# Kernel optimization log

Hardware: AMD Instinct MI355X
Metric: run time of the kernel (lower is better)

The kernel has to match this reference:

```python
import jax, jax.numpy as jnp
import numpy as np

B, S, T, D, K = 8, 500, 30, 5, 10
H, TW, E = 64, 512, 8000


def gru_scan(x, Wi, Wh, bi, bh, lengths=None):
    """Torch-convention GRU. x: [N,T,Din] -> (full [N,T,H], last [N,H]).
    If lengths is given, hidden state freezes past each sequence's length and
    padded steps of `full` are zeroed."""
    N, Tn, _ = x.shape
    Hh = Wh.shape[0]
    xg = jnp.moveaxis(x @ Wi + bi, 1, 0)  # [T,N,3H]

    def step(h, inp):
        xg_t, t = inp
        hg = h @ Wh + bh
        xr, xz, xn = jnp.split(xg_t, 3, axis=-1)
        hr, hz, hn = jnp.split(hg, 3, axis=-1)
        r = jax.nn.sigmoid(xr + hr)
        z = jax.nn.sigmoid(xz + hz)
        n = jnp.tanh(xn + r * hn)
        h_new = (1.0 - z) * n + z * h
        if lengths is not None:
            valid = (t < lengths)[:, None]
            h_new = jnp.where(valid, h_new, h)
            full_t = jnp.where(valid, h_new, 0.0)
        else:
            full_t = h_new
        return h_new, full_t

    h0 = jnp.zeros((N, Hh), x.dtype)
    last, full = jax.lax.scan(step, h0, (xg, jnp.arange(Tn)))
    return jnp.moveaxis(full, 0, 1), last


def layer_norm(x, g, b, eps=1e-5):
    m = jnp.mean(x, axis=-1, keepdims=True)
    v = jnp.var(x, axis=-1, keepdims=True)
    return (x - m) / jnp.sqrt(v + eps) * g + b


def setup_inputs() -> dict:
    key = jax.random.key(0)
    ks = jax.random.split(key, 40)
    p = lambda i, shape: jax.random.normal(ks[i], shape, jnp.float32) * 0.05
    inp = {}
    inp['price'] = jax.random.normal(ks[0], (B, S, T, 3), jnp.float32)
    inp['tweets'] = jax.random.normal(ks[1], (B, S, D, K, TW), jnp.float32)
    inp['tweet_counts'] = jax.random.randint(ks[2], (B, S, D), 0, K + 1, jnp.int32)
    inp['edge_index'] = jax.random.randint(ks[3], (2, E), 0, S, jnp.int32)
    inp['num_edge_type'] = 3
    # price GRU (in=3)
    inp['pg_Wi'] = p(4, (3, 3 * H)); inp['pg_Wh'] = p(5, (H, 3 * H))
    inp['pg_bi'] = p(6, (3 * H,)); inp['pg_bh'] = p(7, (3 * H,))
    # tweet GRU (in=512)
    inp['tg_Wi'] = p(8, (TW, 3 * H)); inp['tg_Wh'] = p(9, (H, 3 * H))
    inp['tg_bi'] = p(10, (3 * H,)); inp['tg_bh'] = p(11, (3 * H,))
    # date GRU (in=64)
    inp['dg_Wi'] = p(12, (H, 3 * H)); inp['dg_Wh'] = p(13, (H, 3 * H))
    inp['dg_bi'] = p(14, (3 * H,)); inp['dg_bh'] = p(15, (3 * H,))
    inp['bil_A'] = p(16, (H, H, H)); inp['bil_b'] = p(17, (H,))
    inp['gnn_W'] = p(18, (H, H)); inp['gnn_b'] = p(19, (H,))
    inp['fc1_W'] = p(20, (2 * H, H)); inp['fc1_b'] = p(21, (H,))
    inp['ln1_g'] = jnp.ones((H,), jnp.float32); inp['ln1_b'] = jnp.zeros((H,), jnp.float32)
    inp['fc2_W'] = p(22, (H, H)); inp['fc2_b'] = p(23, (H,))
    inp['ln2_g'] = jnp.ones((H,), jnp.float32); inp['ln2_b'] = jnp.zeros((H,), jnp.float32)
    inp['mlp_W1'] = p(24, (H, H)); inp['mlp_b1'] = p(25, (H,))
    inp['mlp_W2'] = p(26, (H, 1)); inp['mlp_b2'] = p(27, (1,))
    return inp


def reference(price, tweets, pg_Wi, pg_Wh, pg_bi, pg_bh,
              tg_Wi, tg_Wh, tg_bi, tg_bh, dg_Wi, dg_Wh, dg_bi, dg_bh,
              bil_A, bil_b, gnn_W, gnn_b, fc1_W, fc1_b, ln1_g, ln1_b,
              fc2_W, fc2_b, ln2_g, ln2_b, mlp_W1, mlp_b1, mlp_W2, mlp_b2,
              tweet_counts, edge_index, num_edge_type):
    # NOTE: in the original, attn applies softmax over dim=1 of a [T,1] score,
    # i.e. a size-1 axis, so the weights are identically 1 and the attention
    # context is exactly sum(full, axis=0). We reproduce that exact math.
    # Price branch: GRU over T days for every (window, stock), then masked sum.
    pf, _ = gru_scan(price.reshape(B * S, T, 3), pg_Wi, pg_Wh, pg_bi, pg_bh)
    x = pf.sum(axis=1)  # [B*S, H]

    # Tweet branch: ragged GRU over up to K tweets per (window, stock, date).
    tw = tweets.reshape(B * S * D, K, TW)
    lens = tweet_counts.reshape(B * S * D)
    tf, _ = gru_scan(tw, tg_Wi, tg_Wh, tg_bi, tg_bh, lengths=lens)
    news = tf.sum(axis=1).reshape(B * S, D, H)  # zeros where count==0

    # Date GRU over the D daily news vectors.
    df, _ = gru_scan(news, dg_Wi, dg_Wh, dg_bi, dg_bh)
    text = df.sum(axis=1)  # [B*S, H]

    # Bilinear fusion: out_k = text A_k x + b_k, then tanh.
    comb = jnp.tanh(jnp.einsum('ni,kij,nj->nk', text, bil_A, x) + bil_b)
    ft = comb.reshape(B, S, H)

    # Simple GNN: mean-aggregate neighbor features over edge list, then linear.
    src, dst = edge_index[0], edge_index[1]
    deg = jax.ops.segment_sum(jnp.ones((E,), ft.dtype), dst, num_segments=S)
    denom = jnp.maximum(deg, 1.0)[:, None]
    agg = jax.vmap(lambda m: jax.ops.segment_sum(m, dst, num_segments=S))(ft[:, src, :])
    g = jnp.tanh((agg / denom) @ gnn_W + gnn_b)

    h = jnp.concatenate([ft, g], axis=-1)            # [B,S,2H]
    h = jax.nn.relu(layer_norm(h @ fc1_W + fc1_b, ln1_g, ln1_b))  # dropout: eval
    h = jax.nn.relu(layer_norm(h @ fc2_W + fc2_b, ln2_g, ln2_b))
    h = jax.nn.relu(h @ mlp_W1 + mlp_b1)
    logits = (h @ mlp_W2 + mlp_b2).reshape(B, S)
    return logits
```

## Files before the change

kernel.cpp:

```cpp
#include <hip/hip_runtime.h>
#include <math.h>

#define Bq 8
#define Sq 500
#define Tq 30
#define Dq 5
#define Kq 10
#define Hq 64
#define TWq 512
#define Eq 8000
#define NS (Bq*Sq)
#define NTt (NS*Dq)
#define G3 (3*Hq)
#define TG 4

#define MR 48
#define KC 64
#define XPITCH 72
#define XGP 196
#define NKT (TWq/32)
#define NNT (G3/16)
#define PSEQ 16

#define XROWS 40
#define STG_PLANE (MR*XPITCH)
#define STG_BUF  (2*STG_PLANE)

typedef __attribute__((ext_vector_type(8))) short short8_t;
typedef __attribute__((ext_vector_type(4))) float float4_t;

__device__ __forceinline__ float fsig(float x) {
    return 1.0f / (1.0f + __expf(-x));
}
__device__ __forceinline__ float ftanh(float x) {
    return 1.0f - 2.0f / (__expf(2.0f * x) + 1.0f);
}

__device__ __forceinline__ float wave_sum64(float v) {
    #pragma unroll
    for (int off = 32; off; off >>= 1) v += __shfl_xor(v, off, 64);
    return v;
}

__device__ __forceinline__ short f32_to_bf16_rn(float f) {
    union { float f; unsigned u; } v; v.f = f;
    unsigned r = v.u + 0x7fffu + ((v.u >> 16) & 1u);
    return (short)(r >> 16);
}
__device__ __forceinline__ float bf16_to_f32(short s) {
    union { unsigned u; float f; } v; v.u = ((unsigned)(unsigned short)s) << 16;
    return v.f;
}

__global__ __launch_bounds__(64)
void wfrag_prep_kernel(const float* __restrict__ Wi,
                       short* __restrict__ Wf_hi, short* __restrict__ Wf_lo) {
    const int kt = blockIdx.x / NNT;
    const int nt = blockIdx.x - kt*NNT;
    const int lane = threadIdx.x;
    const int quad = lane >> 4, l16 = lane & 15;
    short h[8], l[8];
    #pragma unroll
    for (int j = 0; j < 8; j++) {
        int k = kt*32 + quad*8 + j;
        int n = nt*16 + l16;
        float w = Wi[(size_t)k*G3 + n];
        short hi = f32_to_bf16_rn(w);
        short lo = f32_to_bf16_rn(w - bf16_to_f32(hi));
        h[j] = hi; l[j] = lo;
    }
    size_t off = ((size_t)blockIdx.x*64 + lane)*8;
    *(short8_t*)(Wf_hi + off) = *(const short8_t*)h;
    *(short8_t*)(Wf_lo + off) = *(const short8_t*)l;
}

__global__ __launch_bounds__(64)
void bilfrag_prep_kernel(const float* __restrict__ A,
                         short* __restrict__ Bf_hi, short* __restrict__ Bf_lo) {
    const int kt = blockIdx.x >> 2;
    const int nt = blockIdx.x & 3;
    const int lane = threadIdx.x;
    const int quad = lane >> 4, l16 = lane & 15;
    short h[8], l[8];
    #pragma unroll
    for (int j = 0; j < 8; j++) {
        int kidx = kt*32 + quad*8 + j;
        int n = nt*16 + l16;
        float w = A[(size_t)n*4096 + kidx];
        short hi = f32_to_bf16_rn(w);
        h[j] = hi; l[j] = f32_to_bf16_rn(w - bf16_to_f32(hi));
    }
    size_t off = ((size_t)blockIdx.x*64 + lane)*8;
    *(short8_t*)(Bf_hi + off) = *(const short8_t*)h;
    *(short8_t*)(Bf_lo + off) = *(const short8_t*)l;
}

__global__ __launch_bounds__(256)
void price_gru_mfma_kernel(const float* __restrict__ price,
                           const float* __restrict__ Wi,
                           const short* __restrict__ Whf_hi, const short* __restrict__ Whf_lo,
                           const float* __restrict__ bi, const float* __restrict__ bh,
                           float* __restrict__ xout) {
    __shared__ __align__(16) float price_s[PSEQ*90];
    __shared__ __align__(16) short h_hi[PSEQ*72];
    __shared__ __align__(16) short h_lo[PSEQ*72];
    const int tid = threadIdx.x;
    const int n0 = blockIdx.x * PSEQ;
    const int wv = tid >> 6;
    const int lane = tid & 63;
    const int quad = lane >> 4;
    const int l16 = lane & 15;
    const int u = wv*16 + l16;
    for (int i = tid; i < PSEQ*90; i += 256) price_s[i] = price[(size_t)n0*90 + i];
    for (int i = tid; i < PSEQ*72; i += 256) { h_hi[i] = 0; h_lo[i] = 0; }
    float wir[3], wiz[3], win[3];
    #pragma unroll
    for (int k = 0; k < 3; k++) {
        wir[k] = Wi[k*G3 + u];
        wiz[k] = Wi[k*G3 + 64 + u];
        win[k] = Wi[k*G3 + 128 + u];
    }
    const float cbr = bi[u] + bh[u];
    const float cbz = bi[64+u] + bh[64+u];
    const float bin = bi[128+u];
    const float bhn = bh[128+u];
    short8_t bfh[2][3], bfl[2][3];
    #pragma unroll
    for (int kt = 0; kt < 2; kt++)
        #pragma unroll
        for (int g = 0; g < 3; g++) {
            size_t off = (((size_t)kt*NNT + (g*4 + wv))*64 + lane)*8;
            bfh[kt][g] = *(const short8_t*)(Whf_hi + off);
            bfl[kt][g] = *(const short8_t*)(Whf_lo + off);
        }
    float hprev[4] = {0.f,0.f,0.f,0.f}, sum[4] = {0.f,0.f,0.f,0.f};
    __syncthreads();
    for (int t = 0; t < Tq; t++) {
        short8_t ah[2], al[2];
        #pragma unroll
        for (int kt = 0; kt < 2; kt++) {
            int addr = l16*72 + kt*32 + quad*8;
            ah[kt] = *(const short8_t*)&h_hi[addr];
            al[kt] = *(const short8_t*)&h_lo[addr];
        }
        float4_t accr = {0.f,0.f,0.f,0.f}, accz = {0.f,0.f,0.f,0.f}, accn = {0.f,0.f,0.f,0.f};
        #pragma unroll
        for (int kt = 0; kt < 2; kt++) {
            accr = __builtin_amdgcn_mfma_f32_16x16x32_bf16(ah[kt], bfh[kt][0], accr, 0,0,0);
            accr = __builtin_amdgcn_mfma_f32_16x16x32_bf16(ah[kt], bfl[kt][0], accr, 0,0,0);
            accr = __builtin_amdgcn_mfma_f32_16x16x32_bf16(al[kt], bfh[kt][0], accr, 0,0,0);
            accz = __builtin_amdgcn_mfma_f32_16x16x32_bf16(ah[kt], bfh[kt][1], accz, 0,0,0);
            accz = __builtin_amdgcn_mfma_f32_16x16x32_bf16(ah[kt], bfl[kt][1], accz, 0,0,0);
            accz = __builtin_amdgcn_mfma_f32_16x16x32_bf16(al[kt], bfh[kt][1], accz, 0,0,0);
            accn = __builtin_amdgcn_mfma_f32_16x16x32_bf16(ah[kt], bfh[kt][2], accn, 0,0,0);
            accn = __builtin_amdgcn_mfma_f32_16x16x32_bf16(ah[kt], bfl[kt][2], accn, 0,0,0);
            accn = __builtin_amdgcn_mfma_f32_16x16x32_bf16(al[kt], bfl[kt][2], accn, 0,0,0);
        }
        __syncthreads();
        #pragma unroll
        for (int r = 0; r < 4; r++) {
            const int s = quad*4 + r;
            float p0 = price_s[s*90 + t*3 + 0];
            float p1 = price_s[s*90 + t*3 + 1];
            float p2 = price_s[s*90 + t*3 + 2];
            float xr = fmaf(p2, wir[2], fmaf(p1, wir[1], fmaf(p0, wir[0], cbr)));
            float xz = fmaf(p2, wiz[2], fmaf(p1, wiz[1], fmaf(p0, wiz[0], cbz)));
            float xn = fmaf(p2, win[2], fmaf(p1, win[1], fmaf(p0, win[0], bin)));
            float rg = fsig(xr + accr[r]);
            float zg = fsig(xz + accz[r]);
            float ng = ftanh(xn + rg*(accn[r] + bhn));
            float h = (1.0f - zg)*ng + zg*hprev[r];
            hprev[r] = h; sum[r] += h;
            short hh = f32_to_bf16_rn(h);
            h_hi[s*72 + u] = hh;
            h_lo[s*72 + u] = f32_to_bf16_rn(h - bf16_to_f32(hh));
        }
        __syncthreads();
    }
    #pragma unroll
    for (int r = 0; r < 4; r++)
        xout[(size_t)(n0 + quad*4 + r)*Hq + u] = sum[r];
}

__global__ __launch_bounds__(256, 4)
void tweet_gru_kernel(const float* __restrict__ tweets,
                      const int* __restrict__ counts,
                      const short* __restrict__ Wf_hi, const short* __restrict__ Wf_lo,
                      const short* __restrict__ Wht_hi, const short* __restrict__ Wht_lo,
                      const float* __restrict__ bi, const float* __restrict__ bh,
                      float* __restrict__ news) {
    __shared__ __align__(16) char smem[XROWS*XGP*4];
    __shared__ __align__(16) short rh_hi[16*72];
    __shared__ __align__(16) short rh_lo[16*72];
    __shared__ int len_s[TG];
    __shared__ int tmax_s;
    short* stg = (short*)smem;
    float* xg  = (float*)smem;

    const int tid  = threadIdx.x;
    const int n0   = blockIdx.x * TG;
    const int wave = tid >> 6;
    const int lane = tid & 63;
    const int quad = lane >> 4;
    const int l16  = lane & 15;

    if (tid < TG) {
        int c = counts[n0 + tid];
        len_s[tid] = c < 0 ? 0 : (c > Kq ? Kq : c);
    }
    for (int i = tid; i < 16*72; i += 256) { rh_hi[i] = 0; rh_lo[i] = 0; }
    __syncthreads();
    if (tid == 0) {
        int m01 = len_s[0] > len_s[1] ? len_s[0] : len_s[1];
        int m23 = len_s[2] > len_s[3] ? len_s[2] : len_s[3];
        tmax_s = m01 > m23 ? m01 : m23;
    }

    const float* gp[3];
    int lofs[3];
    bool val[3];
    #pragma unroll
    for (int j = 0; j < 3; j++) {
        const int ii = tid + j*256;
        const bool ok = ii < TG*Kq*(KC/4);
        const int i = ok ? ii : 0;
        const int row = i >> 4;
        const int c4  = i & 15;
        const int s   = (row*205) >> 11;
        const int t   = row - s*10;
        val[j]  = ok && (t < len_s[s]);
        gp[j]   = tweets + (((size_t)(n0+s))*Kq + t)*TWq + c4*4;
        lofs[j] = row*XPITCH + c4*4;
    }

    float4_t acc[3][3];
    #pragma unroll
    for (int a = 0; a < 3; a++)
        #pragma unroll
        for (int b = 0; b < 3; b++)
            acc[a][b] = (float4_t){0.f, 0.f, 0.f, 0.f};

    #pragma unroll
    for (int j = 0; j < 3; j++) if (val[j]) {
        float4 v = *(const float4*)(gp[j]);
        float f[4] = {v.x, v.y, v.z, v.w};
        short hh[4], ll[4];
        #pragma unroll
        for (int q = 0; q < 4; q++) {
            short hi = f32_to_bf16_rn(f[q]);
            hh[q] = hi;
            ll[q] = f32_to_bf16_rn(f[q] - bf16_to_f32(hi));
        }
        *(short4*)&stg[lofs[j]]             = *(const short4*)hh;
        *(short4*)&stg[STG_PLANE + lofs[j]] = *(const short4*)ll;
    }
    __syncthreads();

    for (int ch = 0; ch < TWq/KC; ch++) {
        const int cur = ch & 1;
        float4 v[3];
        if (ch < TWq/KC - 1) {
            #pragma unroll
            for (int j = 0; j < 3; j++) if (val[j])
                v[j] = *(const float4*)(gp[j] + (ch+1)*KC);
        }
        const short* xh = stg + cur*STG_BUF;
        const short* xl = xh + STG_PLANE;
        #pragma unroll
        for (int ks = 0; ks < KC/32; ks++) {
            const int kt = ch*(KC/32) + ks;
            short8_t bh_[3], bl_[3];
            #pragma unroll
            for (int ntl = 0; ntl < 3; ntl++) {
                size_t off = (((size_t)kt*NNT + (wave*3 + ntl))*64 + lane)*8;
                bh_[ntl] = *(const short8_t*)(Wf_hi + off);
                bl_[ntl] = *(const short8_t*)(Wf_lo + off);
            }
            short8_t ah_[3], al_[3];
            #pragma unroll
            for (int mt = 0; mt < 3; mt++) {
                int addr = (mt*16 + l16)*XPITCH + ks*32 + quad*8;
                ah_[mt] = *(const short8_t*)&xh[addr];
                al_[mt] = *(const short8_t*)&xl[addr];
            }
            #pragma unroll
            for (int mt = 0; mt < 3; mt++)
                #pragma unroll
                for (int ntl = 0; ntl < 3; ntl++) {
                    acc[mt][ntl] = __builtin_amdgcn_mfma_f32_16x16x32_bf16(ah_[mt], bh_[ntl], acc[mt][ntl], 0, 0, 0);
                    acc[mt][ntl] = __builtin_amdgcn_mfma_f32_16x16x32_bf16(ah_[mt], bl_[ntl], acc[mt][ntl], 0, 0, 0);
                    acc[mt][ntl] = __builtin_amdgcn_mfma_f32_16x16x32_bf16(al_[mt], bh_[ntl], acc[mt][ntl], 0, 0, 0);
                }
        }
        if (ch < TWq/KC - 1) {
            short* yh = stg + (cur^1)*STG_BUF;
            short* yl = yh + STG_PLANE;
            #pragma unroll
            for (int j = 0; j < 3; j++) if (val[j]) {
                float f[4] = {v[j].x, v[j].y, v[j].z, v[j].w};
                short hh[4], ll[4];
                #pragma unroll
                for (int q = 0; q < 4; q++) {
                    short hi = f32_to_bf16_rn(f[q]);
                    hh[q] = hi;
                    ll[q] = f32_to_bf16_rn(f[q] - bf16_to_f32(hi));
                }
                *(short4*)&yh[lofs[j]] = *(const short4*)hh;
                *(short4*)&yl[lofs[j]] = *(const short4*)ll;
            }
        }
        __syncthreads();
    }

    #pragma unroll
    for (int ntl = 0; ntl < 3; ntl++) {
        const int col = (wave*3 + ntl)*16 + l16;
        const float bic = bi[col];
        #pragma unroll
        for (int mt = 0; mt < 3; mt++) {
            const int row0 = mt*16 + quad*4;
            if (row0 < XROWS) {
                #pragma unroll
                for (int r2 = 0; r2 < 4; r2++)
                    xg[(row0 + r2)*XGP + col] = acc[mt][ntl][r2] + bic;
            }
        }
    }

    const int u = wave*16 + l16;
    short8_t tbh[2][3], tbl[2][3];
    #pragma unroll
    for (int kt = 0; kt < 2; kt++)
        #pragma unroll
        for (int g = 0; g < 3; g++) {
            size_t off = (((size_t)kt*NNT + (g*4 + wave))*64 + lane)*8;
            tbh[kt][g] = *(const short8_t*)(Wht_hi + off);
            tbl[kt][g] = *(const short8_t*)(Wht_lo + off);
        }
    const float bhr = bh[u];
    const float bhz = bh[64+u];
    const float bhn = bh[128+u];
    int lp[4];
    #pragma unroll
    for (int r = 0; r < 4; r++) lp[r] = len_s[r];
    float hprev[4] = {0.f,0.f,0.f,0.f}, sum[4] = {0.f,0.f,0.f,0.f};
    const int tmax = tmax_s;
    for (int t = 0; t < tmax; t++) {
        const int ha = l16*72;
        short8_t ah0 = *(const short8_t*)&rh_hi[ha + quad*8];
        short8_t ah1 = *(const short8_t*)&rh_hi[ha + 32 + quad*8];
        short8_t al0 = *(const short8_t*)&rh_lo[ha + quad*8];
        short8_t al1 = *(const short8_t*)&rh_lo[ha + 32 + quad*8];
        float4_t ar = {0.f,0.f,0.f,0.f}, az = {0.f,0.f,0.f,0.f}, an = {0.f,0.f,0.f,0.f};
        ar = __builtin_amdgcn_mfma_f32_16x16x32_bf16(ah0, tbh[0][0], ar, 0,0,0);
        ar = __builtin_amdgcn_mfma_f32_16x16x32_bf16(ah0, tbl[0][0], ar, 0,0,0);
        ar = __builtin_amdgcn_mfma_f32_16x16x32_bf16(al0, tbh[0][0], ar, 0,0,0);
        ar = __builtin_amdgcn_mfma_f32_16x16x32_bf16(ah1, tbh[1][0], ar, 0,0,0);
        ar = __builtin_amdgcn_mfma_f32_16x16x32_bf16(ah1, tbl[1][0], ar, 0,0,0);
        ar = __builtin_amdgcn_mfma_f32_16x16x32_bf16(al1, tbh[1][0], ar, 0,0,0);
        az = __builtin_amdgcn_mfma_f32_16x16x32_bf16(ah0, tbh[0][1], az, 0,0,0);
        az = __builtin_amdgcn_mfma_f32_16x16x32_bf16(ah0, tbl[0][1], az, 0,0,0);
        az = __builtin_amdgcn_mfma_f32_16x16x32_bf16(al0, tbh[0][1], az, 0,0,0);
        az = __builtin_amdgcn_mfma_f32_16x16x32_bf16(ah1, tbh[1][1], az, 0,0,0);
        az = __builtin_amdgcn_mfma_f32_16x16x32_bf16(ah1, tbl[1][1], az, 0,0,0);
        az = __builtin_amdgcn_mfma_f32_16x16x32_bf16(al1, tbh[1][1], az, 0,0,0);
        an = __builtin_amdgcn_mfma_f32_16x16x32_bf16(ah0, tbh[0][2], an, 0,0,0);
        an = __builtin_amdgcn_mfma_f32_16x16x32_bf16(ah0, tbl[0][2], an, 0,0,0);
        an = __builtin_amdgcn_mfma_f32_16x16x32_bf16(al0, tbh[0][2], an, 0,0,0);
        an = __builtin_amdgcn_mfma_f32_16x16x32_bf16(ah1, tbh[1][2], an, 0,0,0);
        an = __builtin_amdgcn_mfma_f32_16x16x32_bf16(ah1, tbl[1][2], an, 0,0,0);
        an = __builtin_amdgcn_mfma_f32_16x16x32_bf16(al1, tbl[1][2], an, 0,0,0);
        __syncthreads();
        if (quad == 0) {
            #pragma unroll
            for (int r = 0; r < 4; r++) {
                if (t < lp[r]) {
                    const float* xr = &xg[(r*Kq + t)*XGP];
                    float rg = fsig(xr[u]        + ar[r] + bhr);
                    float zg = fsig(xr[Hq+u]     + az[r] + bhz);
                    float ng = ftanh(xr[2*Hq+u]  + rg*(an[r] + bhn));
                    float hn = (1.0f - zg)*ng + zg*hprev[r];
                    hprev[r] = hn; sum[r] += hn;
                    short hh = f32_to_bf16_rn(hn);
                    rh_hi[r*72 + u] = hh;
                    rh_lo[r*72 + u] = f32_to_bf16_rn(hn - bf16_to_f32(hh));
                }
            }
        }
        __syncthreads();
    }
    if (quad == 0) {
        #pragma unroll
        for (int r = 0; r < 4; r++)
            news[(size_t)(n0 + r)*Hq + u] = sum[r];
    }
}

__global__ __launch_bounds__(192)
void date_gru_kernel(const float* __restrict__ news,
                     const float* __restrict__ Wi, const float* __restrict__ Wh,
                     const float* __restrict__ bi, const float* __restrict__ bh,
                     float* __restrict__ text) {
    __shared__ __align__(16) float nw_s[Dq*Hq];
    __shared__ __align__(16) float h_s[Hq];
    __shared__ __align__(16) float xg_s[G3];
    __shared__ __align__(16) float hg_s[G3];
    const int n = blockIdx.x;
    const int g = threadIdx.x;
    for (int i = g; i < Dq*Hq; i += 192) nw_s[i] = news[(size_t)n*Dq*Hq + i];
    float wi[Hq], wh[Hq];
    #pragma unroll
    for (int j = 0; j < Hq; j++) { wi[j] = Wi[j*G3+g]; wh[j] = Wh[j*G3+g]; }
    const float big = bi[g], bhg = bh[g];
    if (g < Hq) h_s[g] = 0.0f;
    float hreg = 0.0f, sum = 0.0f;
    __syncthreads();
    for (int t = 0; t < Dq; t++) {
        float a0=0.f,a1=0.f,a2=0.f,a3=0.f, b0=0.f,b1=0.f,b2=0.f,b3=0.f;
        #pragma unroll
        for (int j = 0; j < Hq; j += 4) {
            float4 nv = *(const float4*)&nw_s[t*Hq + j];
            float4 hv = *(const float4*)&h_s[j];
            a0 = fmaf(nv.x, wi[j+0], a0);
            a1 = fmaf(nv.y, wi[j+1], a1);
            a2 = fmaf(nv.z, wi[j+2], a2);
            a3 = fmaf(nv.w, wi[j+3], a3);
            b0 = fmaf(hv.x, wh[j+0], b0);
            b1 = fmaf(hv.y, wh[j+1], b1);
            b2 = fmaf(hv.z, wh[j+2], b2);
            b3 = fmaf(hv.w, wh[j+3], b3);
        }
        xg_s[g] = big + ((a0+a1)+(a2+a3));
        hg_s[g] = bhg + ((b0+b1)+(b2+b3));
        __syncthreads();
        if (g < Hq) {
            float r  = fsig(xg_s[g]      + hg_s[g]);
            float z  = fsig(xg_s[Hq+g]   + hg_s[Hq+g]);
            float nn = ftanh(xg_s[2*Hq+g] + r*hg_s[2*Hq+g]);
            hreg = (1.0f - z)*nn + z*hreg;
            sum += hreg;
            h_s[g] = hreg;
        }
        __syncthreads();
    }
    if (g < Hq) text[(size_t)n*Hq + g] = sum;
}

#define TP 68
#define XP 72
__global__ __launch_bounds__(256)
void bilinear_mfma_kernel(const float* __restrict__ text, const float* __restrict__ x,
                          const short* __restrict__ Bf_hi, const short* __restrict__ Bf_lo,
                          const float* __restrict__ bb, float* __restrict__ ft) {
    __shared__ __align__(16) float t_s[16*TP];
    __shared__ __align__(16) float x_s[16*XP];
    const int tid = threadIdx.x;
    const int n0 = blockIdx.x * 16;
    const int wv = tid >> 6, lane = tid & 63, quad = lane >> 4, l16 = lane & 15;
    for (int i = tid; i < 16*64; i += 256) {
        int r = i >> 6, c = i & 63;
        t_s[r*TP + c] = text[(size_t)(n0 + r)*Hq + c];
        x_s[r*XP + c] = x[(size_t)(n0 + r)*Hq + c];
    }
    float4_t acc = {0.f,0.f,0.f,0.f};
    __syncthreads();
    for (int kt = 0; kt < 128; kt++) {
        const int i  = kt >> 1;
        const int j0 = (kt & 1)*32 + quad*8;
        size_t boff = (((size_t)kt*4 + wv)*64 + lane)*8;
        short8_t bh_ = *(const short8_t*)(Bf_hi + boff);
        short8_t bl_ = *(const short8_t*)(Bf_lo + boff);
        float ti = t_s[l16*TP + i];
        float xv[8];
        *(float4*)&xv[0] = *(const float4*)&x_s[l16*XP + j0];
        *(float4*)&xv[4] = *(const float4*)&x_s[l16*XP + j0 + 4];
        short ph[8], pl[8];
        #pragma unroll
        for (int jj = 0; jj < 8; jj++) {
            float p = ti * xv[jj];
            short hi = f32_to_bf16_rn(p);
            ph[jj] = hi;
            pl[jj] = f32_to_bf16_rn(p - bf16_to_f32(hi));
        }
        short8_t ah = *(const short8_t*)ph;
        short8_t al = *(const short8_t*)pl;
        acc = __builtin_amdgcn_mfma_f32_16x16x32_bf16(ah, bh_, acc, 0,0,0);
        acc = __builtin_amdgcn_mfma_f32_16x16x32_bf16(ah, bl_, acc, 0,0,0);
        acc = __builtin_amdgcn_mfma_f32_16x16x32_bf16(al, bh_, acc, 0,0,0);
    }
    const int col = wv*16 + l16;
    const float bk = bb[col];
    #pragma unroll
    for (int r = 0; r < 4; r++) {
        int n = quad*4 + r;
        ft[(size_t)(n0 + n)*Hq + col] = ftanh(acc[r] + bk);
    }
}

__global__ void count_kernel(const int* __restrict__ ei, int* __restrict__ cnt) {
    int e = blockIdx.x*256 + threadIdx.x;
    if (e < Eq) atomicAdd(&cnt[ei[Eq + e]], 1);
}

__global__ __launch_bounds__(512)
void scan_kernel(const int* __restrict__ cnt, int* __restrict__ off,
                 int* __restrict__ cursor) {
    __shared__ int buf[512];
    const int tid = threadIdx.x;
    int v = (tid < Sq) ? cnt[tid] : 0;
    buf[tid] = v;
    __syncthreads();
    #pragma unroll
    for (int d = 1; d < 512; d <<= 1) {
        int t = (tid >= d) ? buf[tid - d] : 0;
        __syncthreads();
        buf[tid] += t;
        __syncthreads();
    }
    if (tid <= Sq) {
        int excl = buf[tid] - v;
        off[tid] = excl;
        if (tid < Sq) cursor[tid] = excl;
    }
}

__global__ void scatter_kernel(const int* __restrict__ ei, int* __restrict__ cursor,
                               int* __restrict__ sorted_src) {
    int e = blockIdx.x*256 + threadIdx.x;
    if (e < Eq) {
        int dst = ei[Eq + e];
        int p = atomicAdd(&cursor[dst], 1);
        sorted_src[p] = ei[e];
    }
}

__global__ __launch_bounds__(64)
void head_kernel(const float* __restrict__ ft,
                 const int* __restrict__ off, const int* __restrict__ sorted_src,
                 const float* __restrict__ gnn_W, const float* __restrict__ gnn_b,
                 const float* __restrict__ fc1_W, const float* __restrict__ fc1_b,
                 const float* __restrict__ ln1_g, const float* __restrict__ ln1_b,
                 const float* __restrict__ fc2_W, const float* __restrict__ fc2_b,
                 const float* __restrict__ ln2_g, const float* __restrict__ ln2_b,
                 const float* __restrict__ mlp_W1, const float* __restrict__ mlp_b1,
                 const float* __restrict__ mlp_W2, const float* __restrict__ mlp_b2,
                 float* __restrict__ out) {
    __shared__ __align__(16) float a_s[Hq];
    __shared__ __align__(16) float in_s[2*Hq];
    __shared__ __align__(16) float t_s[Hq];
    const int n = blockIdx.x;
    const int b = n / Sq;
    const int s = n - b*Sq;
    const int u = threadIdx.x;
    const int o0 = off[s], o1 = off[s+1];
    const float* ftb = ft + (size_t)b*Sq*Hq;
    float acc = 0.0f;
    for (int e = o0; e < o1; ++e)
        acc += ftb[(size_t)sorted_src[e]*Hq + u];
    const float denom = (o1 - o0) > 1 ? (float)(o1 - o0) : 1.0f;
    a_s[u]  = acc / denom;
    in_s[u] = ft[(size_t)n*Hq + u];
    __syncthreads();
    {
        float a0=0.f,a1=0.f,a2=0.f,a3=0.f;
        #pragma unroll
        for (int j = 0; j < Hq; j += 4) {
            a0 = fmaf(a_s[j+0], gnn_W[(j+0)*Hq + u], a0);
            a1 = fmaf(a_s[j+1], gnn_W[(j+1)*Hq + u], a1);
            a2 = fmaf(a_s[j+2], gnn_W[(j+2)*Hq + u], a2);
            a3 = fmaf(a_s[j+3], gnn_W[(j+3)*Hq + u], a3);
        }
        in_s[Hq+u] = ftanh(gnn_b[u] + ((a0+a1)+(a2+a3)));
    }
    __syncthreads();
    float v;
    {
        float a0=0.f,a1=0.f,a2=0.f,a3=0.f;
        #pragma unroll
        for (int j = 0; j < 2*Hq; j += 4) {
            a0 = fmaf(in_s[j+0], fc1_W[(j+0)*Hq + u], a0);
            a1 = fmaf(in_s[j+1], fc1_W[(j+1)*Hq + u], a1);
            a2 = fmaf(in_s[j+2], fc1_W[(j+2)*Hq + u], a2);
            a3 = fmaf(in_s[j+3], fc1_W[(j+3)*Hq + u], a3);
        }
        v = fc1_b[u] + ((a0+a1)+(a2+a3));
        float m = wave_sum64(v) * (1.0f/Hq);
        float d = v - m;
        float var = wave_sum64(d*d) * (1.0f/Hq);
        v = fmaxf(d * rsqrtf(var + 1e-5f) * ln1_g[u] + ln1_b[u], 0.0f);
    }
    t_s[u] = v;
    __syncthreads();
    {
        float a0=0.f,a1=0.f,a2=0.f,a3=0.f;
        #pragma unroll
        for (int j = 0; j < Hq; j += 4) {
            a0 = fmaf(t_s[j+0], fc2_W[(j+0)*Hq + u], a0);
            a1 = fmaf(t_s[j+1], fc2_W[(j+1)*Hq + u], a1);
            a2 = fmaf(t_s[j+2], fc2_W[(j+2)*Hq + u], a2);
            a3 = fmaf(t_s[j+3], fc2_W[(j+3)*Hq + u], a3);
        }
        v = fc2_b[u] + ((a0+a1)+(a2+a3));
        float m = wave_sum64(v) * (1.0f/Hq);
        float d = v - m;
        float var = wave_sum64(d*d) * (1.0f/Hq);
        v = fmaxf(d * rsqrtf(var + 1e-5f) * ln2_g[u] + ln2_b[u], 0.0f);
    }
    __syncthreads();
    a_s[u] = v;
    __syncthreads();
    {
        float a0=0.f,a1=0.f,a2=0.f,a3=0.f;
        #pragma unroll
        for (int j = 0; j < Hq; j += 4) {
            a0 = fmaf(a_s[j+0], mlp_W1[(j+0)*Hq + u], a0);
            a1 = fmaf(a_s[j+1], mlp_W1[(j+1)*Hq + u], a1);
            a2 = fmaf(a_s[j+2], mlp_W1[(j+2)*Hq + u], a2);
            a3 = fmaf(a_s[j+3], mlp_W1[(j+3)*Hq + u], a3);
        }
        v = fmaxf(mlp_b1[u] + ((a0+a1)+(a2+a3)), 0.0f);
    }
    float p = wave_sum64(v * mlp_W2[u]);
    if (u == 0) out[n] = p + mlp_b2[0];
}

extern "C" void kernel_launch(void* const* d_in, const int* in_sizes, int n_in,
                              void* d_out, int out_size, void* d_ws, size_t ws_size,
                              hipStream_t stream) {
    (void)in_sizes; (void)n_in; (void)out_size; (void)ws_size;
    const float* price  = (const float*)d_in[0];
    const float* tweets = (const float*)d_in[1];
    const int*   counts = (const int*)d_in[2];
    const int*   ei     = (const int*)d_in[3];
    const float* pg_Wi = (const float*)d_in[5];
    const float* pg_Wh = (const float*)d_in[6];
    const float* pg_bi = (const float*)d_in[7];
    const float* pg_bh = (const float*)d_in[8];
    const float* tg_Wi = (const float*)d_in[9];
    const float* tg_Wh = (const float*)d_in[10];
    const float* tg_bi = (const float*)d_in[11];
    const float* tg_bh = (const float*)d_in[12];
    const float* dg_Wi = (const float*)d_in[13];
    const float* dg_Wh = (const float*)d_in[14];
    const float* dg_bi = (const float*)d_in[15];
    const float* dg_bh = (const float*)d_in[16];
    const float* bil_A = (const float*)d_in[17];
    const float* bil_b = (const float*)d_in[18];
    const float* gnn_W = (const float*)d_in[19];
    const float* gnn_b = (const float*)d_in[20];
    const float* fc1_W = (const float*)d_in[21];
    const float* fc1_b = (const float*)d_in[22];
    const float* ln1_g = (const float*)d_in[23];
    const float* ln1_b = (const float*)d_in[24];
    const float* fc2_W = (const float*)d_in[25];
    const float* fc2_b = (const float*)d_in[26];
    const float* ln2_g = (const float*)d_in[27];
    const float* ln2_b = (const float*)d_in[28];
    const float* mlp_W1 = (const float*)d_in[29];
    const float* mlp_b1 = (const float*)d_in[30];
    const float* mlp_W2 = (const float*)d_in[31];
    const float* mlp_b2 = (const float*)d_in[32];

    float* ws      = (float*)d_ws;
    float* x_price = ws;
    float* news    = ws + 256000;
    float* text    = ws + 1536000;
    float* ft      = ws + 1792000;
    int*   cnt     = (int*)(ws + 2048000);
    int*   off     = cnt + 512;
    int*   cursor  = off + 512;
    int*   sorted  = cursor + 512;
    short* Wf_hi   = (short*)(ws + 2304512);
    short* Wf_lo   = Wf_hi  + 98304;
    short* Whp_hi  = Wf_lo  + 98304;
    short* Whp_lo  = Whp_hi + 12288;
    short* Bf_hi   = Whp_lo + 12288;
    short* Bf_lo   = Bf_hi  + 262144;
    short* Wht_hi  = Bf_lo  + 262144;
    short* Wht_lo  = Wht_hi + 12288;

    hipMemsetAsync(cnt, 0, 512*sizeof(int), stream);

    count_kernel<<<(Eq+255)/256, 256, 0, stream>>>(ei, cnt);
    scan_kernel<<<1, 512, 0, stream>>>(cnt, off, cursor);
    scatter_kernel<<<(Eq+255)/256, 256, 0, stream>>>(ei, cursor, sorted);

    wfrag_prep_kernel<<<NKT*NNT, 64, 0, stream>>>(tg_Wi, Wf_hi, Wf_lo);
    wfrag_prep_kernel<<<2*NNT, 64, 0, stream>>>(pg_Wh, Whp_hi, Whp_lo);
    wfrag_prep_kernel<<<2*NNT, 64, 0, stream>>>(tg_Wh, Wht_hi, Wht_lo);
    bilfrag_prep_kernel<<<128*4, 64, 0, stream>>>(bil_A, Bf_hi, Bf_lo);

    price_gru_mfma_kernel<<<NS/PSEQ, 256, 0, stream>>>(price, pg_Wi, Whp_hi, Whp_lo,
                                                       pg_bi, pg_bh, x_price);
    tweet_gru_kernel<<<NTt/TG, 256, 0, stream>>>(tweets, counts, Wf_hi, Wf_lo,
                                                 Wht_hi, Wht_lo, tg_bi, tg_bh, news);
    date_gru_kernel<<<NS, 192, 0, stream>>>(news, dg_Wi, dg_Wh, dg_bi, dg_bh, text);
    bilinear_mfma_kernel<<<NS/16, 256, 0, stream>>>(text, x_price, Bf_hi, Bf_lo, bil_b, ft);
    head_kernel<<<NS, 64, 0, stream>>>(ft, off, sorted,
                                       gnn_W, gnn_b, fc1_W, fc1_b, ln1_g, ln1_b,
                                       fc2_W, fc2_b, ln2_g, ln2_b,
                                       mlp_W1, mlp_b1, mlp_W2, mlp_b2,
                                       (float*)d_out);
}
```

Baseline: 848.2 us.

## Compact tweet rows by prefix offsets, skip empty MFMA tiles, merge prep launches

The tweet GRU now packs each sequence's valid tweets contiguously using a per-block prefix sum. M-tiles past the packed row total skip their fragment loads and MFMAs, which removes work on padded tweets. The CSR build (memset, count, scan, scatter) becomes one single-block kernel, and the four weight-fragment prep launches become one kernel, cutting launch overhead. It also corrects the lo*hi term in two n-gate MFMA chains (lo*lo replaced with lo*hi), and it adds an extra barrier in the tweet kernel.

```diff
diff --git a/kernel.cpp b/kernel.cpp
--- a/kernel.cpp
+++ b/kernel.cpp
@@ -26,6 +26,12 @@
 #define STG_PLANE (MR*XPITCH)
 #define STG_BUF  (2*STG_PLANE)
 
+#define PREP_WF   (NKT*NNT)
+#define PREP_WHP  (2*NNT)
+#define PREP_WHT  (2*NNT)
+#define PREP_BIL  512
+#define PREP_BLOCKS (PREP_WF+PREP_WHP+PREP_WHT+PREP_BIL)
+
 typedef __attribute__((ext_vector_type(8))) short short8_t;
 typedef __attribute__((ext_vector_type(4))) float float4_t;
 
@@ -53,46 +59,79 @@
 }
 
 __global__ __launch_bounds__(64)
-void wfrag_prep_kernel(const float* __restrict__ Wi,
-                       short* __restrict__ Wf_hi, short* __restrict__ Wf_lo) {
-    const int kt = blockIdx.x / NNT;
-    const int nt = blockIdx.x - kt*NNT;
+void prep_all_kernel(const float* __restrict__ tg_Wi, const float* __restrict__ pg_Wh,
+                     const float* __restrict__ tg_Wh, const float* __restrict__ bil_A,
+                     short* __restrict__ Wf_hi, short* __restrict__ Wf_lo,
+                     short* __restrict__ Whp_hi, short* __restrict__ Whp_lo,
+                     short* __restrict__ Wht_hi, short* __restrict__ Wht_lo,
+                     short* __restrict__ Bf_hi, short* __restrict__ Bf_lo) {
+    const int bx = blockIdx.x;
     const int lane = threadIdx.x;
     const int quad = lane >> 4, l16 = lane & 15;
     short h[8], l[8];
-    #pragma unroll
-    for (int j = 0; j < 8; j++) {
-        int k = kt*32 + quad*8 + j;
-        int n = nt*16 + l16;
-        float w = Wi[(size_t)k*G3 + n];
-        short hi = f32_to_bf16_rn(w);
-        short lo = f32_to_bf16_rn(w - bf16_to_f32(hi));
-        h[j] = hi; l[j] = lo;
-    }
-    size_t off = ((size_t)blockIdx.x*64 + lane)*8;
-    *(short8_t*)(Wf_hi + off) = *(const short8_t*)h;
-    *(short8_t*)(Wf_lo + off) = *(const short8_t*)l;
-}
-
-__global__ __launch_bounds__(64)
-void bilfrag_prep_kernel(const float* __restrict__ A,
-                         short* __restrict__ Bf_hi, short* __restrict__ Bf_lo) {
-    const int kt = blockIdx.x >> 2;
-    const int nt = blockIdx.x & 3;
-    const int lane = threadIdx.x;
-    const int quad = lane >> 4, l16 = lane & 15;
-    short h[8], l[8];
-    #pragma unroll
-    for (int j = 0; j < 8; j++) {
-        int kidx = kt*32 + quad*8 + j;
-        int n = nt*16 + l16;
-        float w = A[(size_t)n*4096 + kidx];
-        short hi = f32_to_bf16_rn(w);
-        h[j] = hi; l[j] = f32_to_bf16_rn(w - bf16_to_f32(hi));
-    }
-    size_t off = ((size_t)blockIdx.x*64 + lane)*8;
-    *(short8_t*)(Bf_hi + off) = *(const short8_t*)h;
-    *(short8_t*)(Bf_lo + off) = *(const short8_t*)l;
+    if (bx < PREP_WF + PREP_WHP + PREP_WHT) {
+        const float* W; short *dh, *dl; int b;
+        if (bx < PREP_WF)               { W = tg_Wi; dh = Wf_hi;  dl = Wf_lo;  b = bx; }
+        else if (bx < PREP_WF+PREP_WHP) { W = pg_Wh; dh = Whp_hi; dl = Whp_lo; b = bx - PREP_WF; }
+        else                            { W = tg_Wh; dh = Wht_hi; dl = Wht_lo; b = bx - PREP_WF - PREP_WHP; }
+        const int kt = b / NNT;
+        const int nt = b - kt*NNT;
+        #pragma unroll
+        for (int j = 0; j < 8; j++) {
+            float w = W[(size_t)(kt*32 + quad*8 + j)*G3 + nt*16 + l16];
+            short hi = f32_to_bf16_rn(w);
+            h[j] = hi; l[j] = f32_to_bf16_rn(w - bf16_to_f32(hi));
+        }
+        size_t off = ((size_t)b*64 + lane)*8;
+        *(short8_t*)(dh + off) = *(const short8_t*)h;
+        *(short8_t*)(dl + off) = *(const short8_t*)l;
+    } else {
+        const int b = bx - (PREP_WF+PREP_WHP+PREP_WHT);
+        const int kt = b >> 2;
+        const int nt = b & 3;
+        #pragma unroll
+        for (int j = 0; j < 8; j++) {
+            float w = bil_A[(size_t)(nt*16 + l16)*4096 + kt*32 + quad*8 + j];
+            short hi = f32_to_bf16_rn(w);
+            h[j] = hi; l[j] = f32_to_bf16_rn(w - bf16_to_f32(hi));
+        }
+        size_t off = ((size_t)b*64 + lane)*8;
+        *(short8_t*)(Bf_hi + off) = *(const short8_t*)h;
+        *(short8_t*)(Bf_lo + off) = *(const short8_t*)l;
+    }
+}
+
+__global__ __launch_bounds__(512)
+void csr_kernel(const int* __restrict__ ei, int* __restrict__ off,
+                int* __restrict__ sorted_src) {
+    __shared__ int lcnt[512];
+    __shared__ int lbuf[512];
+    const int tid = threadIdx.x;
+    lcnt[tid] = 0;
+    __syncthreads();
+    for (int e = tid; e < Eq; e += 512)
+        atomicAdd(&lcnt[ei[Eq + e]], 1);
+    __syncthreads();
+    int v = lcnt[tid];
+    lbuf[tid] = v;
+    __syncthreads();
+    #pragma unroll
+    for (int d = 1; d < 512; d <<= 1) {
+        int t = (tid >= d) ? lbuf[tid - d] : 0;
+        __syncthreads();
+        lbuf[tid] += t;
+        __syncthreads();
+    }
+    const int excl = lbuf[tid] - v;
+    if (tid <= Sq) off[tid] = excl;
+    __syncthreads();
+    lcnt[tid] = excl;
+    __syncthreads();
+    for (int e = tid; e < Eq; e += 512) {
+        int dst = ei[Eq + e];
+        int p = atomicAdd(&lcnt[dst], 1);
+        sorted_src[p] = ei[e];
+    }
 }
 
 __global__ __launch_bounds__(256)
@@ -154,7 +193,7 @@
             accz = __builtin_amdgcn_mfma_f32_16x16x32_bf16(al[kt], bfh[kt][1], accz, 0,0,0);
             accn = __builtin_amdgcn_mfma_f32_16x16x32_bf16(ah[kt], bfh[kt][2], accn, 0,0,0);
             accn = __builtin_amdgcn_mfma_f32_16x16x32_bf16(ah[kt], bfl[kt][2], accn, 0,0,0);
-            accn = __builtin_amdgcn_mfma_f32_16x16x32_bf16(al[kt], bfl[kt][2], accn, 0,0,0);
+            accn = __builtin_amdgcn_mfma_f32_16x16x32_bf16(al[kt], bfh[kt][2], accn, 0,0,0);
         }
         __syncthreads();
         #pragma unroll
@@ -193,6 +232,7 @@
     __shared__ __align__(16) short rh_hi[16*72];
     __shared__ __align__(16) short rh_lo[16*72];
     __shared__ int len_s[TG];
+    __shared__ int pref_s[TG+1];
     __shared__ int tmax_s;
     short* stg = (short*)smem;
     float* xg  = (float*)smem;
@@ -211,10 +251,17 @@
     for (int i = tid; i < 16*72; i += 256) { rh_hi[i] = 0; rh_lo[i] = 0; }
     __syncthreads();
     if (tid == 0) {
+        int p = 0;
+        #pragma unroll
+        for (int s = 0; s < TG; s++) { pref_s[s] = p; p += len_s[s]; }
+        pref_s[TG] = p;
         int m01 = len_s[0] > len_s[1] ? len_s[0] : len_s[1];
         int m23 = len_s[2] > len_s[3] ? len_s[2] : len_s[3];
         tmax_s = m01 > m23 ? m01 : m23;
     }
+    __syncthreads();
+    const int total = pref_s[TG];
+    const int mt_hi = (total + 15) >> 4;
 
     const float* gp[3];
     int lofs[3];
@@ -230,7 +277,7 @@
         const int t   = row - s*10;
         val[j]  = ok && (t < len_s[s]);
         gp[j]   = tweets + (((size_t)(n0+s))*Kq + t)*TWq + c4*4;
-        lofs[j] = row*XPITCH + c4*4;
+        lofs[j] = (pref_s[s] + t)*XPITCH + c4*4;
     }
 
     float4_t acc[3][3];
@@ -278,13 +325,13 @@
             }
             short8_t ah_[3], al_[3];
             #pragma unroll
-            for (int mt = 0; mt < 3; mt++) {
+            for (int mt = 0; mt < 3; mt++) if (mt < mt_hi) {
                 int addr = (mt*16 + l16)*XPITCH + ks*32 + quad*8;
                 ah_[mt] = *(const short8_t*)&xh[addr];
                 al_[mt] = *(const short8_t*)&xl[addr];
             }
             #pragma unroll
-            for (int mt = 0; mt < 3; mt++)
+            for (int mt = 0; mt < 3; mt++) if (mt < mt_hi)
                 #pragma unroll
                 for (int ntl = 0; ntl < 3; ntl++) {
                     acc[mt][ntl] = __builtin_amdgcn_mfma_f32_16x16x32_bf16(ah_[mt], bh_[ntl], acc[mt][ntl], 0, 0, 0);
@@ -319,11 +366,10 @@
         #pragma unroll
         for (int mt = 0; mt < 3; mt++) {
             const int row0 = mt*16 + quad*4;
-            if (row0 < XROWS) {
-                #pragma unroll
-                for (int r2 = 0; r2 < 4; r2++)
+            #pragma unroll
+            for (int r2 = 0; r2 < 4; r2++)
+                if (row0 + r2 < total)
                     xg[(row0 + r2)*XGP + col] = acc[mt][ntl][r2] + bic;
-            }
         }
     }
 
@@ -340,9 +386,9 @@
     const float bhr = bh[u];
     const float bhz = bh[64+u];
     const float bhn = bh[128+u];
-    int lp[4];
-    #pragma unroll
-    for (int r = 0; r < 4; r++) lp[r] = len_s[r];
+    int lp[4], pr[4];
+    #pragma unroll
+    for (int r = 0; r < 4; r++) { lp[r] = len_s[r]; pr[r] = pref_s[r]; }
     float hprev[4] = {0.f,0.f,0.f,0.f}, sum[4] = {0.f,0.f,0.f,0.f};
     const int tmax = tmax_s;
     for (int t = 0; t < tmax; t++) {
@@ -369,13 +415,13 @@
         an = __builtin_amdgcn_mfma_f32_16x16x32_bf16(al0, tbh[0][2], an, 0,0,0);
         an = __builtin_amdgcn_mfma_f32_16x16x32_bf16(ah1, tbh[1][2], an, 0,0,0);
         an = __builtin_amdgcn_mfma_f32_16x16x32_bf16(ah1, tbl[1][2], an, 0,0,0);
-        an = __builtin_amdgcn_mfma_f32_16x16x32_bf16(al1, tbl[1][2], an, 0,0,0);
+        an = __builtin_amdgcn_mfma_f32_16x16x32_bf16(al1, tbh[1][2], an, 0,0,0);
         __syncthreads();
         if (quad == 0) {
             #pragma unroll
             for (int r = 0; r < 4; r++) {
                 if (t < lp[r]) {
-                    const float* xr = &xg[(r*Kq + t)*XGP];
+                    const float* xr = &xg[(pr[r] + t)*XGP];
                     float rg = fsig(xr[u]        + ar[r] + bhr);
                     float zg = fsig(xr[Hq+u]     + az[r] + bhz);
                     float ng = ftanh(xr[2*Hq+u]  + rg*(an[r] + bhn));
@@ -494,43 +540,6 @@
     for (int r = 0; r < 4; r++) {
         int n = quad*4 + r;
         ft[(size_t)(n0 + n)*Hq + col] = ftanh(acc[r] + bk);
-    }
-}
-
-__global__ void count_kernel(const int* __restrict__ ei, int* __restrict__ cnt) {
-    int e = blockIdx.x*256 + threadIdx.x;
-    if (e < Eq) atomicAdd(&cnt[ei[Eq + e]], 1);
-}
-
-__global__ __launch_bounds__(512)
-void scan_kernel(const int* __restrict__ cnt, int* __restrict__ off,
-                 int* __restrict__ cursor) {
-    __shared__ int buf[512];
-    const int tid = threadIdx.x;
-    int v = (tid < Sq) ? cnt[tid] : 0;
-    buf[tid] = v;
-    __syncthreads();
-    #pragma unroll
-    for (int d = 1; d < 512; d <<= 1) {
-        int t = (tid >= d) ? buf[tid - d] : 0;
-        __syncthreads();
-        buf[tid] += t;
-        __syncthreads();
-    }
-    if (tid <= Sq) {
-        int excl = buf[tid] - v;
-        off[tid] = excl;
-        if (tid < Sq) cursor[tid] = excl;
-    }
-}
-
-__global__ void scatter_kernel(const int* __restrict__ ei, int* __restrict__ cursor,
-                               int* __restrict__ sorted_src) {
-    int e = blockIdx.x*256 + threadIdx.x;
-    if (e < Eq) {
-        int dst = ei[Eq + e];
-        int p = atomicAdd(&cursor[dst], 1);
-        sorted_src[p] = ei[e];
     }
 }
 
@@ -666,10 +675,8 @@
     float* news    = ws + 256000;
     float* text    = ws + 1536000;
     float* ft      = ws + 1792000;
-    int*   cnt     = (int*)(ws + 2048000);
-    int*   off     = cnt + 512;
-    int*   cursor  = off + 512;
-    int*   sorted  = cursor + 512;
+    int*   off     = (int*)(ws + 2048000);
+    int*   sorted  = off + 512;
     short* Wf_hi   = (short*)(ws + 2304512);
     short* Wf_lo   = Wf_hi  + 98304;
     short* Whp_hi  = Wf_lo  + 98304;
@@ -679,16 +686,10 @@
     short* Wht_hi  = Bf_lo  + 262144;
     short* Wht_lo  = Wht_hi + 12288;
 
-    hipMemsetAsync(cnt, 0, 512*sizeof(int), stream);
-
-    count_kernel<<<(Eq+255)/256, 256, 0, stream>>>(ei, cnt);
-    scan_kernel<<<1, 512, 0, stream>>>(cnt, off, cursor);
-    scatter_kernel<<<(Eq+255)/256, 256, 0, stream>>>(ei, cursor, sorted);
-
-    wfrag_prep_kernel<<<NKT*NNT, 64, 0, stream>>>(tg_Wi, Wf_hi, Wf_lo);
-    wfrag_prep_kernel<<<2*NNT, 64, 0, stream>>>(pg_Wh, Whp_hi, Whp_lo);
-    wfrag_prep_kernel<<<2*NNT, 64, 0, stream>>>(tg_Wh, Wht_hi, Wht_lo);
-    bilfrag_prep_kernel<<<128*4, 64, 0, stream>>>(bil_A, Bf_hi, Bf_lo);
+    csr_kernel<<<1, 512, 0, stream>>>(ei, off, sorted);
+    prep_all_kernel<<<PREP_BLOCKS, 64, 0, stream>>>(
+        tg_Wi, pg_Wh, tg_Wh, bil_A,
+        Wf_hi, Wf_lo, Whp_hi, Whp_lo, Wht_hi, Wht_lo, Bf_hi, Bf_lo);
 
     price_gru_mfma_kernel<<<NS/PSEQ, 256, 0, stream>>>(price, pg_Wi, Whp_hi, Whp_lo,
                                                        pg_bi, pg_bh, x_price);
```

Result: no change. 844.3 us (-0.5%).
